# Performance work log

Measured on AMD Instinct MI355X. Metric: run time of the kernel, lower is better.

The kernel has to match this reference:

```python
import jax, jax.numpy as jnp
import numpy as np

N, E, D, B, C = 50000, 800000, 128, 20000, 40
EPS_BN = 1e-3    # keras BatchNormalization default epsilon
EPS_NRM = 1e-12  # keras ops.nn.normalize epsilon
FFN_DIMS = {"pre": (D, D), "c1p": (D, D), "c1u": (2 * D, D), "c2p": (D, D), "c2u": (2 * D, D), "post": (D, D)}


def setup_inputs() -> dict:
    key = jax.random.key(0)
    ks = jax.random.split(key, 8)
    inp = {
        "node_features": jax.random.normal(ks[0], (N, D), jnp.float32),
        "edges": jax.random.randint(ks[1], (2, E), 0, N, dtype=jnp.int32),
        "edge_w": jax.random.uniform(ks[2], (E,), jnp.float32),
        "input_node_idx": jax.random.randint(ks[3], (B,), 0, N, dtype=jnp.int32),
    }
    for i, (name, (din, dout)) in enumerate(FFN_DIMS.items()):
        kw = jax.random.fold_in(key, 100 + i)
        inp[name + "_g"] = jnp.ones((din,), jnp.float32)
        inp[name + "_be"] = jnp.zeros((din,), jnp.float32)
        inp[name + "_mu"] = jnp.zeros((din,), jnp.float32)
        inp[name + "_var"] = jnp.ones((din,), jnp.float32)
        inp[name + "_w"] = jax.random.normal(kw, (din, dout), jnp.float32) * (1.0 / float(np.sqrt(din)))
        inp[name + "_bi"] = jnp.zeros((dout,), jnp.float32)
    inp["logits_w"] = jax.random.normal(ks[4], (D, C), jnp.float32) * (1.0 / float(np.sqrt(D)))
    inp["logits_b"] = jnp.zeros((C,), jnp.float32)
    return inp


def ffn(x, g, be, mu, var, w, bi):
    # BatchNorm (inference running stats) -> Dropout (identity) -> Dense + exact gelu
    xn = (x - mu) * jax.lax.rsqrt(var + EPS_BN) * g + be
    return jax.nn.gelu(xn @ w + bi, approximate=False)


def l2norm(x):
    n = jnp.sqrt(jnp.sum(x * x, axis=-1, keepdims=True))
    return x / jnp.maximum(n, EPS_NRM)


def graph_conv(x, node_idx, nbr_idx, ew, prep, upd):
    # gather neighbours -> prepare FFN -> edge-weighted -> segment_sum (reduce='sum')
    msgs = ffn(x[nbr_idx], *prep) * ew[:, None]                         # [E, D]
    red = jax.ops.segment_sum(msgs, node_idx, num_segments=x.shape[0])  # [N, D]
    h = jnp.concatenate([x, red], axis=1)                               # [N, 2D] (combination='concat')
    return l2norm(ffn(h, *upd))                                         # normalize=True


def reference(node_features, edges, edge_w, input_node_idx,
              pre_g, pre_be, pre_mu, pre_var, pre_w, pre_bi,
              c1p_g, c1p_be, c1p_mu, c1p_var, c1p_w, c1p_bi,
              c1u_g, c1u_be, c1u_mu, c1u_var, c1u_w, c1u_bi,
              c2p_g, c2p_be, c2p_mu, c2p_var, c2p_w, c2p_bi,
              c2u_g, c2u_be, c2u_mu, c2u_var, c2u_w, c2u_bi,
              post_g, post_be, post_mu, post_var, post_w, post_bi,
              logits_w, logits_b):
    ew = edge_w / jnp.sum(edge_w)                       # edge_W normalized at init
    node_idx, nbr_idx = edges[0], edges[1]
    x = ffn(node_features, pre_g, pre_be, pre_mu, pre_var, pre_w, pre_bi)
    x = graph_conv(x, node_idx, nbr_idx, ew,
                   (c1p_g, c1p_be, c1p_mu, c1p_var, c1p_w, c1p_bi),
                   (c1u_g, c1u_be, c1u_mu, c1u_var, c1u_w, c1u_bi)) + x
    x = graph_conv(x, node_idx, nbr_idx, ew,
                   (c2p_g, c2p_be, c2p_mu, c2p_var, c2p_w, c2p_bi),
                   (c2u_g, c2u_be, c2u_mu, c2u_var, c2u_w, c2u_bi)) + x
    x = ffn(x, post_g, post_be, post_mu, post_var, post_w, post_bi)
    return x[input_node_idx] @ logits_w + logits_b      # [B, C]
```

## Files before the change

### kernel.cpp

```cpp
#include <hip/hip_runtime.h>
#include <hip/hip_fp16.h>
#include <math.h>

static constexpr int D = 128;
static constexpr float EPS_BN = 1e-3f;

typedef short short8 __attribute__((ext_vector_type(8)));
typedef short short4v __attribute__((ext_vector_type(4)));
typedef float float4v __attribute__((ext_vector_type(4)));

__device__ __forceinline__ float gelu_exact(float x) {
    return 0.5f * x * (1.0f + erff(x * 0.70710678118654752f));
}

__device__ __forceinline__ void f32_to_hilo(float f, short& h, short& l) {
    unsigned u = __float_as_uint(f);
    h = (short)(u >> 16);
    float hf = __uint_as_float(u & 0xFFFF0000u);
    unsigned lu = __float_as_uint(f - hf);
    l = (short)(lu >> 16);
}

__global__ void k_sum(const float* __restrict__ w, int n, float* __restrict__ out) {
    float s = 0.f;
    for (int i = blockIdx.x * blockDim.x + threadIdx.x; i < n; i += gridDim.x * blockDim.x)
        s += w[i];
    for (int off = 32; off > 0; off >>= 1) s += __shfl_down(s, off, 64);
    __shared__ float sm[4];
    int lane = threadIdx.x & 63, wv = threadIdx.x >> 6;
    if (lane == 0) sm[wv] = s;
    __syncthreads();
    if (threadIdx.x == 0) atomicAdd(out, sm[0] + sm[1] + sm[2] + sm[3]);
}

struct FoldArgs {
    const float* g[6]; const float* be[6]; const float* mu[6];
    const float* var[6]; const float* w[6]; const float* bi[6];
    short* wh[6]; short* wl[6]; float* bp[6]; int K[6];
};

__global__ void k_fold_all(FoldArgs fa) {
    const int f = blockIdx.y;
    const int c = blockIdx.x;
    const int K = fa.K[f];
    const float* g = fa.g[f]; const float* be = fa.be[f];
    const float* mu = fa.mu[f]; const float* var = fa.var[f];
    const float* w = fa.w[f]; const float* bi = fa.bi[f];
    short* wh = fa.wh[f]; short* wl = fa.wl[f]; float* bp = fa.bp[f];
    float part = 0.f;
    for (int k = threadIdx.x; k < K; k += blockDim.x) {
        float a = g[k] / sqrtf(var[k] + EPS_BN);
        float wv = w[k * D + c];
        float prod = a * wv;
        short hh, ll;
        f32_to_hilo(prod, hh, ll);
        wh[c * K + k] = hh;
        wl[c * K + k] = ll;
        part += (be[k] - mu[k] * a) * wv;
    }
    for (int off = 32; off > 0; off >>= 1) part += __shfl_down(part, off, 64);
    __shared__ float sm[4];
    int lane = threadIdx.x & 63, wv_ = threadIdx.x >> 6;
    if (lane == 0) sm[wv_] = part;
    __syncthreads();
    if (threadIdx.x == 0) bp[c] = bi[c] + sm[0] + sm[1] + sm[2] + sm[3];
}

__global__ void k_hist(const int* __restrict__ edges, int* __restrict__ cnt, int E) {
    int e = blockIdx.x * blockDim.x + threadIdx.x;
    if (e < E) atomicAdd(&cnt[edges[e]], 1);
}

__global__ void k_scan1(const int* __restrict__ cnt, int* __restrict__ rowptr,
                        int* __restrict__ bsum, int N) {
    __shared__ int sm[1024];
    int t = threadIdx.x;
    int i = blockIdx.x * 1024 + t;
    int c = (i < N) ? cnt[i] : 0;
    sm[t] = c;
    __syncthreads();
    #pragma unroll
    for (int off = 1; off < 1024; off <<= 1) {
        int v = (t >= off) ? sm[t - off] : 0;
        __syncthreads();
        sm[t] += v;
        __syncthreads();
    }
    if (i < N) rowptr[i] = sm[t] - c;
    if (t == 1023) bsum[blockIdx.x] = sm[1023];
}

__global__ void k_scan2(int* __restrict__ bsum, int* __restrict__ bpre,
                        int* __restrict__ rowptr, int nb, int N) {
    int lane = threadIdx.x;
    int v = (lane < nb) ? bsum[lane] : 0;
    #pragma unroll
    for (int off = 1; off < 64; off <<= 1) {
        int u = __shfl_up(v, off, 64);
        if (lane >= off) v += u;
    }
    if (lane < nb) bpre[lane] = v;
    if (lane == nb - 1) rowptr[N] = v;
}

__global__ void k_scan3(int* __restrict__ rowptr, int* __restrict__ pos,
                        const int* __restrict__ bpre, int N) {
    int i = blockIdx.x * 1024 + threadIdx.x;
    if (i >= N) return;
    int off = (blockIdx.x > 0) ? bpre[blockIdx.x - 1] : 0;
    int r = rowptr[i] + off;
    rowptr[i] = r;
    pos[i] = r;
}

__global__ void k_fill(const int* __restrict__ edges, const float* __restrict__ ew,
                       const float* __restrict__ sums, int* __restrict__ pos,
                       int2* __restrict__ cw, int E) {
    int e = blockIdx.x * blockDim.x + threadIdx.x;
    if (e >= E) return;
    float inv = 1.0f / sums[0];
    int dst = edges[e], src = edges[E + e];
    int idx = atomicAdd(&pos[dst], 1);
    int2 v;
    v.x = src;
    v.y = __float_as_int(ew[e] * inv);
    cw[idx] = v;
}

__global__ void k_reduce(const int* __restrict__ rowptr, const int2* __restrict__ cw,
                         const __half* __restrict__ y, float* __restrict__ red, int N) {
    int n = blockIdx.x * (blockDim.x >> 6) + (threadIdx.x >> 6);
    if (n >= N) return;
    int lane = threadIdx.x & 63;
    int sub = lane >> 4;
    int q = lane & 15;
    int start = rowptr[n], end = rowptr[n + 1];
    float acc[8] = {0.f, 0.f, 0.f, 0.f, 0.f, 0.f, 0.f, 0.f};
    int i = start + sub;
    if (i < end) {
        int2 c = cw[i];
        for (;;) {
            int ni = i + 4;
            int2 nc = {0, 0};
            if (ni < end) nc = cw[ni];
            float w = __int_as_float(c.y);
            float4 raw = *((const float4*)(y + (size_t)c.x * D) + q);
            const __half2* hp = (const __half2*)&raw;
            #pragma unroll
            for (int t = 0; t < 4; t++) {
                float2 f = __half22float2(hp[t]);
                acc[t * 2]     += w * f.x;
                acc[t * 2 + 1] += w * f.y;
            }
            if (ni >= end) break;
            i = ni; c = nc;
        }
    }
    #pragma unroll
    for (int t = 0; t < 8; t++) {
        acc[t] += __shfl_xor(acc[t], 16, 64);
        acc[t] += __shfl_xor(acc[t], 32, 64);
    }
    if (sub == 0) {
        float4 o0 = {acc[0], acc[1], acc[2], acc[3]};
        float4 o1 = {acc[4], acc[5], acc[6], acc[7]};
        *((float4*)(red + (size_t)n * D + q * 8)) = o0;
        *((float4*)(red + (size_t)n * D + q * 8 + 4)) = o1;
    }
}

template<int K, bool L2RES, bool OUT16>
__global__ __launch_bounds__(256, 2) void k_ffn(
    const float* __restrict__ A0, const float* __restrict__ A1,
    const short* __restrict__ Wh, const short* __restrict__ Wl,
    const float* __restrict__ bp, const float* __restrict__ resid,
    float* __restrict__ outf, __half* __restrict__ outh, int nrows)
{
    __shared__ short Abuf[2][128][72];
    __shared__ short Wbuf[2][128][72];
    __shared__ float rs[128][2];

    const int tid = threadIdx.x;
    const int lane = tid & 63;
    const int wv = tid >> 6;
    const int wr = wv >> 1;
    const int wc = wv & 1;
    const int m = lane & 15;
    const int quad = lane >> 4;
    const int rowBlock = blockIdx.x * 128;

    float4v acc[4][4];
    #pragma unroll
    for (int ti = 0; ti < 4; ti++)
        #pragma unroll
        for (int tj = 0; tj < 4; tj++)
            acc[ti][tj] = (float4v){0.f, 0.f, 0.f, 0.f};

    for (int cc = 0; cc < K / 64; cc++) {
        const float* Asrc = (K == 256 && cc >= 2) ? A1 : A0;
        const int kb = (K == 256) ? ((cc & 1) * 64) : (cc * 64);
        const int kw = cc * 64;

        #pragma unroll
        for (int t = 0; t < 8; t++) {
            int i = tid + t * 256;
            int r = i >> 4, k4 = i & 15;
            int grow = rowBlock + r; if (grow >= nrows) grow = nrows - 1;
            float4 f = *((const float4*)(Asrc + (size_t)grow * D + kb) + k4);
            short h0, l0, h1, l1, h2, l2, h3, l3;
            f32_to_hilo(f.x, h0, l0);
            f32_to_hilo(f.y, h1, l1);
            f32_to_hilo(f.z, h2, l2);
            f32_to_hilo(f.w, h3, l3);
            short4v hh = {h0, h1, h2, h3};
            short4v ll = {l0, l1, l2, l3};
            *(short4v*)&Abuf[0][r][k4 * 4] = hh;
            *(short4v*)&Abuf[1][r][k4 * 4] = ll;
        }
        #pragma unroll
        for (int t = 0; t < 4; t++) {
            int i = tid + t * 256;
            int c = i >> 3, g = i & 7;
            short8 wh8 = *(const short8*)(Wh + (size_t)c * K + kw + g * 8);
            short8 wl8 = *(const short8*)(Wl + (size_t)c * K + kw + g * 8);
            *(short8*)&Wbuf[0][c][g * 8] = wh8;
            *(short8*)&Wbuf[1][c][g * 8] = wl8;
        }
        __syncthreads();

        #pragma unroll
        for (int ks = 0; ks < 2; ks++) {
            short8 ah[4], al[4], bh[4], bl[4];
            #pragma unroll
            for (int ti = 0; ti < 4; ti++) {
                ah[ti] = *(const short8*)&Abuf[0][wr * 64 + ti * 16 + m][ks * 32 + quad * 8];
                al[ti] = *(const short8*)&Abuf[1][wr * 64 + ti * 16 + m][ks * 32 + quad * 8];
            }
            #pragma unroll
            for (int tj = 0; tj < 4; tj++) {
                bh[tj] = *(const short8*)&Wbuf[0][wc * 64 + tj * 16 + m][ks * 32 + quad * 8];
                bl[tj] = *(const short8*)&Wbuf[1][wc * 64 + tj * 16 + m][ks * 32 + quad * 8];
            }
            #pragma unroll
            for (int ti = 0; ti < 4; ti++)
                #pragma unroll
                for (int tj = 0; tj < 4; tj++) {
                    acc[ti][tj] = __builtin_amdgcn_mfma_f32_16x16x32_bf16(al[ti], bh[tj], acc[ti][tj], 0, 0, 0);
                    acc[ti][tj] = __builtin_amdgcn_mfma_f32_16x16x32_bf16(ah[ti], bl[tj], acc[ti][tj], 0, 0, 0);
                    acc[ti][tj] = __builtin_amdgcn_mfma_f32_16x16x32_bf16(ah[ti], bh[tj], acc[ti][tj], 0, 0, 0);
                }
        }
        __syncthreads();
    }

    float bvv[4];
    #pragma unroll
    for (int tj = 0; tj < 4; tj++) bvv[tj] = bp[wc * 64 + tj * 16 + m];

    float g[4][4][4];
    #pragma unroll
    for (int ti = 0; ti < 4; ti++)
        #pragma unroll
        for (int tj = 0; tj < 4; tj++)
            #pragma unroll
            for (int r4 = 0; r4 < 4; r4++)
                g[ti][tj][r4] = gelu_exact(acc[ti][tj][r4] + bvv[tj]);

    if (L2RES) {
        #pragma unroll
        for (int ti = 0; ti < 4; ti++)
            #pragma unroll
            for (int r4 = 0; r4 < 4; r4++) {
                float ss = 0.f;
                #pragma unroll
                for (int tj = 0; tj < 4; tj++) ss += g[ti][tj][r4] * g[ti][tj][r4];
                ss += __shfl_xor(ss, 1, 64);
                ss += __shfl_xor(ss, 2, 64);
                ss += __shfl_xor(ss, 4, 64);
                ss += __shfl_xor(ss, 8, 64);
                if (m == 0) rs[wr * 64 + ti * 16 + quad * 4 + r4][wc] = ss;
            }
        __syncthreads();
        #pragma unroll
        for (int ti = 0; ti < 4; ti++)
            #pragma unroll
            for (int r4 = 0; r4 < 4; r4++) {
                int rib = wr * 64 + ti * 16 + quad * 4 + r4;
                float tot = rs[rib][0] + rs[rib][1];
                float inv = 1.0f / fmaxf(sqrtf(tot), 1e-12f);
                int row = rowBlock + rib;
                if (row < nrows) {
                    #pragma unroll
                    for (int tj = 0; tj < 4; tj++) {
                        int c = wc * 64 + tj * 16 + m;
                        outf[(size_t)row * D + c] = g[ti][tj][r4] * inv + resid[(size_t)row * D + c];
                    }
                }
            }
    } else {
        #pragma unroll
        for (int ti = 0; ti < 4; ti++)
            #pragma unroll
            for (int r4 = 0; r4 < 4; r4++) {
                int row = rowBlock + wr * 64 + ti * 16 + quad * 4 + r4;
                if (row < nrows) {
                    #pragma unroll
                    for (int tj = 0; tj < 4; tj++) {
                        int c = wc * 64 + tj * 16 + m;
                        if (OUT16) outh[(size_t)row * D + c] = __float2half(g[ti][tj][r4]);
                        else       outf[(size_t)row * D + c] = g[ti][tj][r4];
                    }
                }
            }
    }
}

__global__ void k_logits(const float* __restrict__ x, const int* __restrict__ idx,
                         const float* __restrict__ LW, const float* __restrict__ lb,
                         float* __restrict__ out, int B) {
    int wid = blockIdx.x * 4 + (threadIdx.x >> 6);
    int lane = threadIdx.x & 63;
    if (wid >= B) return;
    int row = __builtin_amdgcn_readfirstlane(idx[wid]);
    if (lane >= 40) return;
    float acc = lb[lane];
    const float4* xr = (const float4*)(x + (size_t)row * D);
    #pragma unroll 4
    for (int k4 = 0; k4 < 32; k4++) {
        float4 xv = xr[k4];
        acc += xv.x * LW[(4 * k4 + 0) * 40 + lane];
        acc += xv.y * LW[(4 * k4 + 1) * 40 + lane];
        acc += xv.z * LW[(4 * k4 + 2) * 40 + lane];
        acc += xv.w * LW[(4 * k4 + 3) * 40 + lane];
    }
    out[(size_t)wid * 40 + lane] = acc;
}

extern "C" void kernel_launch(void* const* d_in, const int* in_sizes, int n_in,
                              void* d_out, int out_size, void* d_ws, size_t ws_size,
                              hipStream_t stream) {
    const float* node_features = (const float*)d_in[0];
    const int*   edges         = (const int*)d_in[1];
    const float* edge_w        = (const float*)d_in[2];
    const int*   input_idx     = (const int*)d_in[3];
    const int N = in_sizes[0] / D;
    const int E = in_sizes[2];
    const int B = in_sizes[3];

    const float* P[6][6];
    for (int f = 0; f < 6; f++)
        for (int q = 0; q < 6; q++)
            P[f][q] = (const float*)d_in[4 + f * 6 + q];
    const float* logits_w = (const float*)d_in[40];
    const float* logits_b = (const float*)d_in[41];

    float* ws = (float*)d_ws;
    size_t nd = (size_t)N * D;
    float* xA  = ws;
    float* y   = ws + nd;
    float* red = ws + 2 * nd;
    float* p   = ws + 3 * nd;
    __half* yh = (__half*)p; p += nd / 2;
    const int Ks[6] = {128, 128, 256, 128, 256, 128};
    short* Wh[6]; short* Wl[6]; float* Bp[6];
    {
        short* sp = (short*)p;
        for (int f = 0; f < 6; f++) {
            Wh[f] = sp; sp += (size_t)Ks[f] * D;
            Wl[f] = sp; sp += (size_t)Ks[f] * D;
        }
        p = (float*)sp;
    }
    for (int f = 0; f < 6; f++) { Bp[f] = p; p += D; }
    int* rowptr = (int*)p; p += (N + 1);
    int* pos    = (int*)p; p += N;
    int* cnt    = (int*)p; p += N;
    float* sums = p; p += 2;
    int* bsum   = (int*)p; p += 64;
    int* bpre   = (int*)p; p += 64;
    int2* cw    = (int2*)p; p += 2 * (size_t)E;

    hipMemsetAsync(cnt, 0, ((size_t)N + 2) * sizeof(int), stream);
    k_sum<<<512, 256, 0, stream>>>(edge_w, E, sums);

    FoldArgs fa;
    for (int f = 0; f < 6; f++) {
        fa.g[f] = P[f][0]; fa.be[f] = P[f][1]; fa.mu[f] = P[f][2];
        fa.var[f] = P[f][3]; fa.w[f] = P[f][4]; fa.bi[f] = P[f][5];
        fa.wh[f] = Wh[f]; fa.wl[f] = Wl[f]; fa.bp[f] = Bp[f]; fa.K[f] = Ks[f];
    }
    k_fold_all<<<dim3(D, 6), 256, 0, stream>>>(fa);

    const int nb = (N + 1023) / 1024;
    k_hist<<<(E + 255) / 256, 256, 0, stream>>>(edges, cnt, E);
    k_scan1<<<nb, 1024, 0, stream>>>(cnt, rowptr, bsum, N);
    k_scan2<<<1, 64, 0, stream>>>(bsum, bpre, rowptr, nb, N);
    k_scan3<<<nb, 1024, 0, stream>>>(rowptr, pos, bpre, N);
    k_fill<<<(E + 255) / 256, 256, 0, stream>>>(edges, edge_w, sums, pos, cw, E);

    const int gb = (N + 127) / 128;
    const int rb = (N + 3) / 4;

    k_ffn<128, false, false><<<gb, 256, 0, stream>>>(node_features, nullptr, Wh[0], Wl[0], Bp[0], nullptr, xA, nullptr, N);
    k_ffn<128, false, true><<<gb, 256, 0, stream>>>(xA, nullptr, Wh[1], Wl[1], Bp[1], nullptr, nullptr, yh, N);
    k_reduce<<<rb, 256, 0, stream>>>(rowptr, cw, yh, red, N);
    k_ffn<256, true, false><<<gb, 256, 0, stream>>>(xA, red, Wh[2], Wl[2], Bp[2], xA, y, nullptr, N);
    k_ffn<128, false, true><<<gb, 256, 0, stream>>>(y, nullptr, Wh[3], Wl[3], Bp[3], nullptr, nullptr, yh, N);
    k_reduce<<<rb, 256, 0, stream>>>(rowptr, cw, yh, red, N);
    k_ffn<256, true, false><<<gb, 256, 0, stream>>>(y, red, Wh[4], Wl[4], Bp[4], y, xA, nullptr, N);
    k_ffn<128, false, false><<<gb, 256, 0, stream>>>(xA, nullptr, Wh[5], Wl[5], Bp[5], nullptr, y, nullptr, N);
    k_logits<<<(B + 3) / 4, 256, 0, stream>>>(y, input_idx, logits_w, logits_b, (float*)d_out, B);
}
```

Baseline: 495.5 us.

## Pack CSR edge entries into 32-bit src|fp16 weight and fuse histogram with sum

Merges the edge-weight sum and destination histogram into one pass over the edges. When N fits in 16 bits, each CSR entry becomes a single 32-bit word holding the source index and an fp16 raw weight, and the normalization by the weight sum moves into the reduce kernel. This halves the CSR bytes read in both reduce passes and drops one kernel launch. The cost is fp16 rounding of the edge weights, which loses precision, and a wider fallback path for large N.

```diff
diff --git a/kernel.cpp b/kernel.cpp
--- a/kernel.cpp
+++ b/kernel.cpp
@@ -21,16 +21,20 @@
     l = (short)(lu >> 16);
 }
 
-__global__ void k_sum(const float* __restrict__ w, int n, float* __restrict__ out) {
+__global__ void k_hist_sum(const int* __restrict__ edges, const float* __restrict__ ew,
+                           int* __restrict__ cnt, float* __restrict__ sums, int E) {
+    int e = blockIdx.x * blockDim.x + threadIdx.x;
     float s = 0.f;
-    for (int i = blockIdx.x * blockDim.x + threadIdx.x; i < n; i += gridDim.x * blockDim.x)
-        s += w[i];
+    if (e < E) {
+        atomicAdd(&cnt[edges[e]], 1);
+        s = ew[e];
+    }
     for (int off = 32; off > 0; off >>= 1) s += __shfl_down(s, off, 64);
     __shared__ float sm[4];
     int lane = threadIdx.x & 63, wv = threadIdx.x >> 6;
     if (lane == 0) sm[wv] = s;
     __syncthreads();
-    if (threadIdx.x == 0) atomicAdd(out, sm[0] + sm[1] + sm[2] + sm[3]);
+    if (threadIdx.x == 0) atomicAdd(sums, sm[0] + sm[1] + sm[2] + sm[3]);
 }
 
 struct FoldArgs {
@@ -66,11 +70,6 @@
     if (threadIdx.x == 0) bp[c] = bi[c] + sm[0] + sm[1] + sm[2] + sm[3];
 }
 
-__global__ void k_hist(const int* __restrict__ edges, int* __restrict__ cnt, int E) {
-    int e = blockIdx.x * blockDim.x + threadIdx.x;
-    if (e < E) atomicAdd(&cnt[edges[e]], 1);
-}
-
 __global__ void k_scan1(const int* __restrict__ cnt, int* __restrict__ rowptr,
                         int* __restrict__ bsum, int N) {
     __shared__ int sm[1024];
@@ -113,24 +112,34 @@
     pos[i] = r;
 }
 
-__global__ void k_fill(const int* __restrict__ edges, const float* __restrict__ ew,
-                       const float* __restrict__ sums, int* __restrict__ pos,
-                       int2* __restrict__ cw, int E) {
+__global__ void k_fill_p(const int* __restrict__ edges, const float* __restrict__ ew,
+                         int* __restrict__ pos, unsigned* __restrict__ cw, int E) {
     int e = blockIdx.x * blockDim.x + threadIdx.x;
     if (e >= E) return;
-    float inv = 1.0f / sums[0];
+    int dst = edges[e], src = edges[E + e];
+    __half h = __float2half(ew[e]);
+    unsigned short wb = __half_as_ushort(h);
+    int idx = atomicAdd(&pos[dst], 1);
+    cw[idx] = ((unsigned)src << 16) | (unsigned)wb;
+}
+
+__global__ void k_fill_w(const int* __restrict__ edges, const float* __restrict__ ew,
+                         int* __restrict__ pos, int2* __restrict__ cw2, int E) {
+    int e = blockIdx.x * blockDim.x + threadIdx.x;
+    if (e >= E) return;
     int dst = edges[e], src = edges[E + e];
     int idx = atomicAdd(&pos[dst], 1);
-    int2 v;
-    v.x = src;
-    v.y = __float_as_int(ew[e] * inv);
-    cw[idx] = v;
-}
-
-__global__ void k_reduce(const int* __restrict__ rowptr, const int2* __restrict__ cw,
+    int2 v; v.x = src; v.y = __float_as_int(ew[e]);
+    cw2[idx] = v;
+}
+
+template<bool PACKED>
+__global__ void k_reduce(const int* __restrict__ rowptr, const unsigned* __restrict__ cw,
+                         const int2* __restrict__ cw2, const float* __restrict__ sums,
                          const __half* __restrict__ y, float* __restrict__ red, int N) {
     int n = blockIdx.x * (blockDim.x >> 6) + (threadIdx.x >> 6);
     if (n >= N) return;
+    float inv = 1.0f / sums[0];
     int lane = threadIdx.x & 63;
     int sub = lane >> 4;
     int q = lane & 15;
@@ -138,13 +147,21 @@
     float acc[8] = {0.f, 0.f, 0.f, 0.f, 0.f, 0.f, 0.f, 0.f};
     int i = start + sub;
     if (i < end) {
-        int2 c = cw[i];
+        unsigned c; int2 c2;
+        if (PACKED) c = cw[i]; else c2 = cw2[i];
         for (;;) {
             int ni = i + 4;
-            int2 nc = {0, 0};
-            if (ni < end) nc = cw[ni];
-            float w = __int_as_float(c.y);
-            float4 raw = *((const float4*)(y + (size_t)c.x * D) + q);
+            unsigned nc = 0; int2 nc2 = {0, 0};
+            if (ni < end) { if (PACKED) nc = cw[ni]; else nc2 = cw2[ni]; }
+            int src; float w;
+            if (PACKED) {
+                src = (int)(c >> 16);
+                w = __half2float(__ushort_as_half((unsigned short)(c & 0xFFFFu))) * inv;
+            } else {
+                src = c2.x;
+                w = __int_as_float(c2.y) * inv;
+            }
+            float4 raw = *((const float4*)(y + (size_t)src * D) + q);
             const __half2* hp = (const __half2*)&raw;
             #pragma unroll
             for (int t = 0; t < 4; t++) {
@@ -153,7 +170,7 @@
                 acc[t * 2 + 1] += w * f.y;
             }
             if (ni >= end) break;
-            i = ni; c = nc;
+            i = ni; c = nc; c2 = nc2;
         }
     }
     #pragma unroll
@@ -378,10 +395,13 @@
     float* sums = p; p += 2;
     int* bsum   = (int*)p; p += 64;
     int* bpre   = (int*)p; p += 64;
-    int2* cw    = (int2*)p; p += 2 * (size_t)E;
+    unsigned* cw = (unsigned*)p; p += E;
+    int2* cw2   = (int2*)p; p += 2 * (size_t)E;
+
+    const bool packed = (N <= 65536);
 
     hipMemsetAsync(cnt, 0, ((size_t)N + 2) * sizeof(int), stream);
-    k_sum<<<512, 256, 0, stream>>>(edge_w, E, sums);
+    k_hist_sum<<<(E + 255) / 256, 256, 0, stream>>>(edges, edge_w, cnt, sums, E);
 
     FoldArgs fa;
     for (int f = 0; f < 6; f++) {
@@ -392,21 +412,25 @@
     k_fold_all<<<dim3(D, 6), 256, 0, stream>>>(fa);
 
     const int nb = (N + 1023) / 1024;
-    k_hist<<<(E + 255) / 256, 256, 0, stream>>>(edges, cnt, E);
     k_scan1<<<nb, 1024, 0, stream>>>(cnt, rowptr, bsum, N);
     k_scan2<<<1, 64, 0, stream>>>(bsum, bpre, rowptr, nb, N);
     k_scan3<<<nb, 1024, 0, stream>>>(rowptr, pos, bpre, N);
-    k_fill<<<(E + 255) / 256, 256, 0, stream>>>(edges, edge_w, sums, pos, cw, E);
+    if (packed)
+        k_fill_p<<<(E + 255) / 256, 256, 0, stream>>>(edges, edge_w, pos, cw, E);
+    else
+        k_fill_w<<<(E + 255) / 256, 256, 0, stream>>>(edges, edge_w, pos, cw2, E);
 
     const int gb = (N + 127) / 128;
     const int rb = (N + 3) / 4;
 
     k_ffn<128, false, false><<<gb, 256, 0, stream>>>(node_features, nullptr, Wh[0], Wl[0], Bp[0], nullptr, xA, nullptr, N);
     k_ffn<128, false, true><<<gb, 256, 0, stream>>>(xA, nullptr, Wh[1], Wl[1], Bp[1], nullptr, nullptr, yh, N);
-    k_reduce<<<rb, 256, 0, stream>>>(rowptr, cw, yh, red, N);
+    if (packed) k_reduce<true><<<rb, 256, 0, stream>>>(rowptr, cw, nullptr, sums, yh, red, N);
+    else        k_reduce<false><<<rb, 256, 0, stream>>>(rowptr, nullptr, cw2, sums, yh, red, N);
     k_ffn<256, true, false><<<gb, 256, 0, stream>>>(xA, red, Wh[2], Wl[2], Bp[2], xA, y, nullptr, N);
     k_ffn<128, false, true><<<gb, 256, 0, stream>>>(y, nullptr, Wh[3], Wl[3], Bp[3], nullptr, nullptr, yh, N);
-    k_reduce<<<rb, 256, 0, stream>>>(rowptr, cw, yh, red, N);
+    if (packed) k_reduce<true><<<rb, 256, 0, stream>>>(rowptr, cw, nullptr, sums, yh, red, N);
+    else        k_reduce<false><<<rb, 256, 0, stream>>>(rowptr, nullptr, cw2, sums, yh, red, N);
     k_ffn<256, true, false><<<gb, 256, 0, stream>>>(y, red, Wh[4], Wl[4], Bp[4], y, xA, nullptr, N);
     k_ffn<128, false, false><<<gb, 256, 0, stream>>>(xA, nullptr, Wh[5], Wl[5], Bp[5], nullptr, y, nullptr, N);
     k_logits<<<(B + 3) / 4, 256, 0, stream>>>(y, input_idx, logits_w, logits_b, (float*)d_out, B);
```

New measurement: 490.3 us. No clear change (-1.0%).
